# Optimization experiments

Measured on AMD Instinct MI355X. Metric: run time of the kernel, lower is better.

## Reference

```python
import jax, jax.numpy as jnp
import numpy as np

N = 100_000      # nodes
E = 3_200_000    # edges (avg degree 32)
D_IN = 128
D_H = 128
EPS = 1e-12      # F.normalize eps


def setup_inputs() -> dict:
    key = jax.random.key(0)
    k1, k2, k3 = jax.random.split(key, 3)
    X = jax.random.normal(k1, (N, D_IN), dtype=jnp.float32)
    edge_index = jax.random.randint(k2, (2, E), 0, N, dtype=jnp.int32)
    # GCNConv linear weight (stored as [in, out] for X @ W) and bias
    W = jax.random.normal(k3, (D_IN, D_H), dtype=jnp.float32) / np.sqrt(D_IN)
    b = jnp.zeros((D_H,), dtype=jnp.float32)
    # MessageNorm learnable scale, init 1.0
    scale = jnp.ones((1,), dtype=jnp.float32)
    return {"X": X, "edge_index": edge_index, "W": W, "b": b, "scale": scale}


def reference(X, edge_index, W, b, scale):
    n = X.shape[0]
    loop = jnp.arange(n, dtype=edge_index.dtype)
    src = jnp.concatenate([edge_index[0], loop])  # add self loops
    tgt = jnp.concatenate([edge_index[1], loop])
    # symmetric GCN normalization: D^{-1/2} (A+I) D^{-1/2}
    deg = jax.ops.segment_sum(jnp.ones_like(src, X.dtype), tgt, num_segments=n)
    dinv = jnp.where(deg > 0, jax.lax.rsqrt(deg), 0.0)
    norm = dinv[src] * dinv[tgt]  # [E+N]
    XW = X @ W  # [N, D_H]
    msg = jax.ops.segment_sum(norm[:, None] * XW[src], tgt, num_segments=n) + b
    # MessageNorm(learn_scale=True): l2-normalize msg, rescale by ||x||_2 * scale
    msg_n = msg / jnp.maximum(jnp.linalg.norm(msg, axis=-1, keepdims=True), EPS)
    x_norm = jnp.linalg.norm(X, axis=-1, keepdims=True)
    return jax.nn.gelu(msg_n * x_norm * scale, approximate=False)
```

## Files before the change

### kernel.cpp

```cpp
#include <hip/hip_runtime.h>
#include <math.h>

#define D 128
#define NB 391
#define BSH 8
#define BMASK 255
#define CAP 10240
#define EPB 4096
#define LDA 136

typedef unsigned short ushort_t;
typedef unsigned int uint_t;
typedef __attribute__((ext_vector_type(8))) short bfrag;
typedef __attribute__((ext_vector_type(4))) float ffrag;

__device__ inline ushort_t f2bf(float f) {
    uint_t u = __float_as_uint(f);
    uint_t r = (u + 0x7FFFu + ((u >> 16) & 1u)) >> 16;
    return (ushort_t)r;
}

__global__ __launch_bounds__(256) void k_bin(const int* __restrict__ src,
                                             const int* __restrict__ tgt, int e,
                                             int* __restrict__ bucket_cur,
                                             uint_t* __restrict__ binned,
                                             const float* __restrict__ W,
                                             ushort_t* __restrict__ Wt) {
    __shared__ uint_t sval[EPB];
    __shared__ ushort_t sbkt[EPB];
    __shared__ int lcnt[NB];
    __shared__ int lbeg[NB];
    __shared__ int gbase[NB];
    __shared__ int pscan[256];
    int tid = threadIdx.x;

    if (blockIdx.x < 16) {
        int nrow = blockIdx.x * 8 + (tid >> 5);
        int k0 = (tid & 31) * 4;
        ushort4 o;
        o.x = f2bf(W[(size_t)(k0 + 0) * D + nrow]);
        o.y = f2bf(W[(size_t)(k0 + 1) * D + nrow]);
        o.z = f2bf(W[(size_t)(k0 + 2) * D + nrow]);
        o.w = f2bf(W[(size_t)(k0 + 3) * D + nrow]);
        *(ushort4*)&Wt[(size_t)nrow * D + k0] = o;
    }

    int base = blockIdx.x * EPB;
    for (int i = tid; i < NB; i += 256) lcnt[i] = 0;
    __syncthreads();

    int myb[16];
    uint_t myval[16];
#pragma unroll
    for (int k = 0; k < 16; ++k) {
        int i = base + k * 256 + tid;
        if (i < e) {
            int t = tgt[i];
            int s = src[i];
            myb[k] = t >> BSH;
            myval[k] = ((uint_t)s << BSH) | (uint_t)(t & BMASK);
            atomicAdd(&lcnt[myb[k]], 1);
        } else {
            myb[k] = -1;
        }
    }
    __syncthreads();

    int c0 = (2 * tid < NB) ? lcnt[2 * tid] : 0;
    int c1 = (2 * tid + 1 < NB) ? lcnt[2 * tid + 1] : 0;
    int x = c0 + c1;
    pscan[tid] = x;
    __syncthreads();
    for (int off = 1; off < 256; off <<= 1) {
        int y = (tid >= off) ? pscan[tid - off] : 0;
        __syncthreads();
        x += y;
        pscan[tid] = x;
        __syncthreads();
    }
    int pb = x - (c0 + c1);
    if (2 * tid < NB) lbeg[2 * tid] = pb;
    if (2 * tid + 1 < NB) lbeg[2 * tid + 1] = pb + c0;
    __syncthreads();

    for (int i = tid; i < NB; i += 256) {
        int c = lcnt[i];
        gbase[i] = (c > 0) ? atomicAdd(&bucket_cur[i], c) : 0;
        lcnt[i] = lbeg[i];
    }
    __syncthreads();

#pragma unroll
    for (int k = 0; k < 16; ++k) {
        if (myb[k] >= 0) {
            int r = atomicAdd(&lcnt[myb[k]], 1);
            sval[r] = myval[k];
            sbkt[r] = (ushort_t)myb[k];
        }
    }
    __syncthreads();

    int nb = min(e - base, EPB);
    for (int i = tid; i < nb; i += 256) {
        int b = sbkt[i];
        int slot = gbase[b] + (i - lbeg[b]);
        if (slot < CAP) binned[(size_t)b * CAP + slot] = sval[i];
    }
}

__global__ __launch_bounds__(256) void k_sort(const uint_t* __restrict__ binned,
                                              const int* __restrict__ bucket_cur,
                                              int* __restrict__ col,
                                              int* __restrict__ rowptr,
                                              float* __restrict__ dinv, int n) {
    __shared__ uint_t sout[CAP];
    __shared__ int scnt[256];
    __shared__ int sincl[256];
    __shared__ int sofs[256];
    __shared__ int sred[256];
    int b = blockIdx.x;
    int tid = threadIdx.x;

    int v = 0;
    for (int i = tid; i < b; i += 256) v += min(bucket_cur[i], CAP);
    sred[tid] = v;
    __syncthreads();
    for (int off = 128; off >= 1; off >>= 1) {
        if (tid < off) sred[tid] += sred[tid + off];
        __syncthreads();
    }
    int baseg = sred[0];

    int nb = min(bucket_cur[b], CAP);
    const uint_t* bin = binned + (size_t)b * CAP;

    scnt[tid] = 0;
    __syncthreads();
    for (int i = tid; i < nb; i += 256)
        atomicAdd(&scnt[bin[i] & BMASK], 1);
    __syncthreads();
    int x = scnt[tid];
    sincl[tid] = x;
    __syncthreads();
    for (int off = 1; off < 256; off <<= 1) {
        int y = (tid >= off) ? sincl[tid - off] : 0;
        __syncthreads();
        x += y;
        sincl[tid] = x;
        __syncthreads();
    }
    sofs[tid] = x - scnt[tid];
    int t = (b << BSH) + tid;
    if (t < n) {
        rowptr[t + 1] = baseg + x;
        dinv[t] = rsqrtf((float)scnt[tid] + 1.0f);
    }
    if (b == 0 && tid == 0) rowptr[0] = 0;
    __syncthreads();
    for (int i = tid; i < nb; i += 256) {
        uint_t w = bin[i];
        int r = atomicAdd(&sofs[w & BMASK], 1);
        sout[r] = w >> BSH;
    }
    __syncthreads();
    for (int i = tid; i < nb; i += 256)
        col[baseg + i] = (int)sout[i];
}

__global__ __launch_bounds__(256) void k_gemm(const float* __restrict__ X,
                                              const ushort_t* __restrict__ Wt,
                                              const float* __restrict__ dinv,
                                              ushort_t* __restrict__ Y,
                                              float* __restrict__ xnorm, int n) {
    __shared__ ushort_t As[64 * LDA];
    __shared__ ushort_t Bs[128 * LDA];
    int tid = threadIdx.x;
    int row0 = blockIdx.x * 64;

    for (int i = tid; i < 128 * 16; i += 256) {
        int nr = i >> 4, c = (i & 15) << 3;
        *(uint4*)&Bs[nr * LDA + c] = *(const uint4*)&Wt[(size_t)nr * D + c];
    }

    const float4* X4 = (const float4*)X;
#pragma unroll
    for (int i2 = 0; i2 < 8; ++i2) {
        int item = i2 * 256 + tid;
        int r = item >> 5, c4 = item & 31;
        int gr = row0 + r;
        float4 v = (gr < n) ? X4[(size_t)gr * 32 + c4] : make_float4(0.f, 0.f, 0.f, 0.f);
        ushort4 bv;
        bv.x = f2bf(v.x); bv.y = f2bf(v.y); bv.z = f2bf(v.z); bv.w = f2bf(v.w);
        *(ushort4*)&As[r * LDA + c4 * 4] = bv;
        float s = v.x * v.x + v.y * v.y + v.z * v.z + v.w * v.w;
        s += __shfl_xor(s, 1);
        s += __shfl_xor(s, 2);
        s += __shfl_xor(s, 4);
        s += __shfl_xor(s, 8);
        s += __shfl_xor(s, 16);
        if ((tid & 31) == 0 && gr < n) xnorm[gr] = sqrtf(s);
    }
    __syncthreads();

    int w = tid >> 6;
    int lane = tid & 63;
    int q = lane >> 4;
    int mi = lane & 15;

    bfrag xf[4];
#pragma unroll
    for (int kt = 0; kt < 4; ++kt)
        xf[kt] = *(const bfrag*)&As[(w * 16 + mi) * LDA + kt * 32 + q * 8];

    ffrag acc[8];
#pragma unroll
    for (int nt = 0; nt < 8; ++nt) acc[nt] = (ffrag){0.f, 0.f, 0.f, 0.f};

#pragma unroll
    for (int nt = 0; nt < 8; ++nt) {
#pragma unroll
        for (int kt = 0; kt < 4; ++kt) {
            bfrag wf = *(const bfrag*)&Bs[(nt * 16 + mi) * LDA + kt * 32 + q * 8];
            acc[nt] = __builtin_amdgcn_mfma_f32_16x16x32_bf16(wf, xf[kt], acc[nt], 0, 0, 0);
        }
    }

    __syncthreads();
    int gr = row0 + w * 16 + mi;
    float dv = (gr < n) ? dinv[gr] : 0.f;
#pragma unroll
    for (int nt = 0; nt < 8; ++nt) {
        ushort4 o;
        o.x = f2bf(acc[nt][0] * dv);
        o.y = f2bf(acc[nt][1] * dv);
        o.z = f2bf(acc[nt][2] * dv);
        o.w = f2bf(acc[nt][3] * dv);
        *(ushort4*)&As[(w * 16 + mi) * LDA + nt * 16 + q * 4] = o;
    }
    __syncthreads();

    int row = tid >> 2, seg = tid & 3;
    int grow = row0 + row;
    if (grow < n) {
#pragma unroll
        for (int k2 = 0; k2 < 4; ++k2) {
            uint4 vv = *(const uint4*)&As[row * LDA + seg * 32 + k2 * 8];
            *(uint4*)&Y[(size_t)grow * D + seg * 32 + k2 * 8] = vv;
        }
    }
}

__global__ __launch_bounds__(256) void k_agg(const ushort_t* __restrict__ Y,
                                             const float* __restrict__ xnorm,
                                             const float* __restrict__ dinv,
                                             const int* __restrict__ rowptr,
                                             const int* __restrict__ col,
                                             const float* __restrict__ bias,
                                             const float* __restrict__ scale,
                                             float* __restrict__ out, int n) {
    int t = (blockIdx.x * 256 + threadIdx.x) >> 6;
    int lane = threadIdx.x & 63;
    if (t >= n) return;

    const char* Yb = (const char*)Y;
    uint_t lo4 = (uint_t)lane * 4;

    uint_t p = *(const uint_t*)(Yb + (((uint_t)t << 8) + lo4));
    float a0 = __uint_as_float(p << 16);
    float a1 = __uint_as_float(p & 0xFFFF0000u);

    int beg = rowptr[t];
    int end = rowptr[t + 1];
    for (int base = beg; base < end; base += 64) {
        int m = min(end - base, 64);
        uint_t cv = (uint_t)col[base + min(lane, m - 1)];
        int k = 0;
        for (; k + 16 <= m; k += 16) {
            uint_t qv[16];
#pragma unroll
            for (int j = 0; j < 16; ++j) {
                uint_t s = (uint_t)__builtin_amdgcn_readlane((int)cv, k + j);
                qv[j] = *(const uint_t*)(Yb + ((size_t)s << 8) + lo4);
            }
#pragma unroll
            for (int j = 0; j < 16; ++j) {
                a0 += __uint_as_float(qv[j] << 16);
                a1 += __uint_as_float(qv[j] & 0xFFFF0000u);
            }
        }
        for (; k + 4 <= m; k += 4) {
            uint_t qv[4];
#pragma unroll
            for (int j = 0; j < 4; ++j) {
                uint_t s = (uint_t)__builtin_amdgcn_readlane((int)cv, k + j);
                qv[j] = *(const uint_t*)(Yb + ((size_t)s << 8) + lo4);
            }
#pragma unroll
            for (int j = 0; j < 4; ++j) {
                a0 += __uint_as_float(qv[j] << 16);
                a1 += __uint_as_float(qv[j] & 0xFFFF0000u);
            }
        }
        for (; k < m; ++k) {
            uint_t s = (uint_t)__builtin_amdgcn_readlane((int)cv, k);
            uint_t q = *(const uint_t*)(Yb + ((size_t)s << 8) + lo4);
            a0 += __uint_as_float(q << 16);
            a1 += __uint_as_float(q & 0xFFFF0000u);
        }
    }

    float dt = dinv[t];
    float m0 = fmaf(dt, a0, bias[lane * 2]);
    float m1 = fmaf(dt, a1, bias[lane * 2 + 1]);

    float m2 = m0 * m0 + m1 * m1;
#pragma unroll
    for (int m = 32; m >= 1; m >>= 1) m2 += __shfl_xor(m2, m);

    float denom = fmaxf(sqrtf(m2), 1e-12f);
    float fac = xnorm[t] * scale[0] / denom;
    float g0 = m0 * fac;
    float g1 = m1 * fac;
    float2 o;
    o.x = 0.5f * g0 * (1.0f + erff(g0 * 0.70710678118654752440f));
    o.y = 0.5f * g1 * (1.0f + erff(g1 * 0.70710678118654752440f));
    *(float2*)&out[(size_t)t * D + lane * 2] = o;
}


extern "C" void kernel_launch(void* const* d_in, const int* in_sizes, int n_in,
                              void* d_out, int out_size, void* d_ws, size_t ws_size,
                              hipStream_t stream) {
    const float* X     = (const float*)d_in[0];
    const int*   ei    = (const int*)d_in[1];
    const float* W     = (const float*)d_in[2];
    const float* bias  = (const float*)d_in[3];
    const float* scale = (const float*)d_in[4];
    float* out = (float*)d_out;

    int n = in_sizes[0] / D;
    int e = in_sizes[1] / 2;
    const int* src = ei;
    const int* tgt = ei + e;

    char* ws = (char*)d_ws;
    ushort_t* Y = (ushort_t*)ws;   ws += (size_t)n * D * sizeof(ushort_t);
    uint_t* binned = (uint_t*)Y;
    float* dinv = (float*)ws;      ws += (size_t)n * sizeof(float);
    float* xnorm = (float*)ws;     ws += (size_t)n * sizeof(float);
    int* rowptr = (int*)ws;        ws += (size_t)(n + 1) * sizeof(int);
    int* bucket_cur = (int*)ws;    ws += NB * sizeof(int);
    int* col = (int*)ws;           ws += (size_t)e * sizeof(int);
    ushort_t* Wt = (ushort_t*)ws;

    hipMemsetAsync(bucket_cur, 0, NB * sizeof(int), stream);
    k_bin<<<(e + EPB - 1) / EPB, 256, 0, stream>>>(src, tgt, e, bucket_cur, binned, W, Wt);
    k_sort<<<NB, 256, 0, stream>>>(binned, bucket_cur, col, rowptr, dinv, n);
    k_gemm<<<(n + 63) / 64, 256, 0, stream>>>(X, Wt, dinv, Y, xnorm, n);
    k_agg<<<(n + 3) / 4, 256, 0, stream>>>(Y, xnorm, dinv, rowptr, col, bias, scale, out, n);
}
```

Before: 305.9 us.

## Fuse bucket sort and GEMM into one launch, move dinv scaling into aggregation

Merges the per-bucket CSR sort and the X@W GEMM into one kernel, with blocks split by index, so the two independent stages run concurrently and one launch is saved. Because the GEMM no longer waits for dinv, the source-side normalization moves into the aggregation loop as an extra per-edge dinv gather. The global prefix-sum over buckets is dropped: sorted columns are written back in place within each fixed-capacity bucket slice, and each row's begin and end are packed as 16-bit offsets into one int. The cost is an extra random dinv load per edge, a separate binned buffer instead of aliasing Y, and a smaller per-bucket capacity that could overflow on skewed degrees.

```diff
diff --git a/kernel.cpp b/kernel.cpp
--- a/kernel.cpp
+++ b/kernel.cpp
@@ -5,7 +5,7 @@
 #define NB 391
 #define BSH 8
 #define BMASK 255
-#define CAP 10240
+#define CAP 9216
 #define EPB 4096
 #define LDA 136
 
@@ -108,144 +108,130 @@
     }
 }
 
-__global__ __launch_bounds__(256) void k_sort(const uint_t* __restrict__ binned,
-                                              const int* __restrict__ bucket_cur,
-                                              int* __restrict__ col,
-                                              int* __restrict__ rowptr,
-                                              float* __restrict__ dinv, int n) {
-    __shared__ uint_t sout[CAP];
-    __shared__ int scnt[256];
-    __shared__ int sincl[256];
-    __shared__ int sofs[256];
-    __shared__ int sred[256];
-    int b = blockIdx.x;
+__global__ __launch_bounds__(256) void k_mid(uint_t* __restrict__ binned,
+                                             const int* __restrict__ bucket_cur,
+                                             int* __restrict__ rowinfo,
+                                             float* __restrict__ dinv,
+                                             const float* __restrict__ X,
+                                             const ushort_t* __restrict__ Wt,
+                                             ushort_t* __restrict__ Y,
+                                             float* __restrict__ xnorm, int n) {
+    __shared__ __align__(16) char smem[52224];
     int tid = threadIdx.x;
 
-    int v = 0;
-    for (int i = tid; i < b; i += 256) v += min(bucket_cur[i], CAP);
-    sred[tid] = v;
-    __syncthreads();
-    for (int off = 128; off >= 1; off >>= 1) {
-        if (tid < off) sred[tid] += sred[tid + off];
-        __syncthreads();
-    }
-    int baseg = sred[0];
-
-    int nb = min(bucket_cur[b], CAP);
-    const uint_t* bin = binned + (size_t)b * CAP;
-
-    scnt[tid] = 0;
-    __syncthreads();
-    for (int i = tid; i < nb; i += 256)
-        atomicAdd(&scnt[bin[i] & BMASK], 1);
-    __syncthreads();
-    int x = scnt[tid];
-    sincl[tid] = x;
-    __syncthreads();
-    for (int off = 1; off < 256; off <<= 1) {
-        int y = (tid >= off) ? sincl[tid - off] : 0;
-        __syncthreads();
-        x += y;
+    if (blockIdx.x < NB) {
+        uint_t* sout = (uint_t*)smem;
+        int* scnt  = (int*)(smem + CAP * 4);
+        int* sincl = scnt + 256;
+        int* sofs  = sincl + 256;
+        int b = blockIdx.x;
+
+        int nb = min(bucket_cur[b], CAP);
+        uint_t* bin = binned + (size_t)b * CAP;
+
+        scnt[tid] = 0;
+        __syncthreads();
+        for (int i = tid; i < nb; i += 256)
+            atomicAdd(&scnt[bin[i] & BMASK], 1);
+        __syncthreads();
+        int x = scnt[tid];
         sincl[tid] = x;
         __syncthreads();
-    }
-    sofs[tid] = x - scnt[tid];
-    int t = (b << BSH) + tid;
-    if (t < n) {
-        rowptr[t + 1] = baseg + x;
-        dinv[t] = rsqrtf((float)scnt[tid] + 1.0f);
-    }
-    if (b == 0 && tid == 0) rowptr[0] = 0;
-    __syncthreads();
-    for (int i = tid; i < nb; i += 256) {
-        uint_t w = bin[i];
-        int r = atomicAdd(&sofs[w & BMASK], 1);
-        sout[r] = w >> BSH;
-    }
-    __syncthreads();
-    for (int i = tid; i < nb; i += 256)
-        col[baseg + i] = (int)sout[i];
-}
-
-__global__ __launch_bounds__(256) void k_gemm(const float* __restrict__ X,
-                                              const ushort_t* __restrict__ Wt,
-                                              const float* __restrict__ dinv,
-                                              ushort_t* __restrict__ Y,
-                                              float* __restrict__ xnorm, int n) {
-    __shared__ ushort_t As[64 * LDA];
-    __shared__ ushort_t Bs[128 * LDA];
-    int tid = threadIdx.x;
-    int row0 = blockIdx.x * 64;
-
-    for (int i = tid; i < 128 * 16; i += 256) {
-        int nr = i >> 4, c = (i & 15) << 3;
-        *(uint4*)&Bs[nr * LDA + c] = *(const uint4*)&Wt[(size_t)nr * D + c];
-    }
-
-    const float4* X4 = (const float4*)X;
-#pragma unroll
-    for (int i2 = 0; i2 < 8; ++i2) {
-        int item = i2 * 256 + tid;
-        int r = item >> 5, c4 = item & 31;
-        int gr = row0 + r;
-        float4 v = (gr < n) ? X4[(size_t)gr * 32 + c4] : make_float4(0.f, 0.f, 0.f, 0.f);
-        ushort4 bv;
-        bv.x = f2bf(v.x); bv.y = f2bf(v.y); bv.z = f2bf(v.z); bv.w = f2bf(v.w);
-        *(ushort4*)&As[r * LDA + c4 * 4] = bv;
-        float s = v.x * v.x + v.y * v.y + v.z * v.z + v.w * v.w;
-        s += __shfl_xor(s, 1);
-        s += __shfl_xor(s, 2);
-        s += __shfl_xor(s, 4);
-        s += __shfl_xor(s, 8);
-        s += __shfl_xor(s, 16);
-        if ((tid & 31) == 0 && gr < n) xnorm[gr] = sqrtf(s);
-    }
-    __syncthreads();
-
-    int w = tid >> 6;
-    int lane = tid & 63;
-    int q = lane >> 4;
-    int mi = lane & 15;
-
-    bfrag xf[4];
-#pragma unroll
-    for (int kt = 0; kt < 4; ++kt)
-        xf[kt] = *(const bfrag*)&As[(w * 16 + mi) * LDA + kt * 32 + q * 8];
-
-    ffrag acc[8];
-#pragma unroll
-    for (int nt = 0; nt < 8; ++nt) acc[nt] = (ffrag){0.f, 0.f, 0.f, 0.f};
-
-#pragma unroll
-    for (int nt = 0; nt < 8; ++nt) {
-#pragma unroll
-        for (int kt = 0; kt < 4; ++kt) {
-            bfrag wf = *(const bfrag*)&Bs[(nt * 16 + mi) * LDA + kt * 32 + q * 8];
-            acc[nt] = __builtin_amdgcn_mfma_f32_16x16x32_bf16(wf, xf[kt], acc[nt], 0, 0, 0);
-        }
-    }
-
-    __syncthreads();
-    int gr = row0 + w * 16 + mi;
-    float dv = (gr < n) ? dinv[gr] : 0.f;
-#pragma unroll
-    for (int nt = 0; nt < 8; ++nt) {
-        ushort4 o;
-        o.x = f2bf(acc[nt][0] * dv);
-        o.y = f2bf(acc[nt][1] * dv);
-        o.z = f2bf(acc[nt][2] * dv);
-        o.w = f2bf(acc[nt][3] * dv);
-        *(ushort4*)&As[(w * 16 + mi) * LDA + nt * 16 + q * 4] = o;
-    }
-    __syncthreads();
-
-    int row = tid >> 2, seg = tid & 3;
-    int grow = row0 + row;
-    if (grow < n) {
-#pragma unroll
-        for (int k2 = 0; k2 < 4; ++k2) {
-            uint4 vv = *(const uint4*)&As[row * LDA + seg * 32 + k2 * 8];
-            *(uint4*)&Y[(size_t)grow * D + seg * 32 + k2 * 8] = vv;
+        for (int off = 1; off < 256; off <<= 1) {
+            int y = (tid >= off) ? sincl[tid - off] : 0;
+            __syncthreads();
+            x += y;
+            sincl[tid] = x;
+            __syncthreads();
+        }
+        sofs[tid] = x - scnt[tid];
+        int t = (b << BSH) + tid;
+        if (t < n) {
+            rowinfo[t] = ((x - scnt[tid]) << 16) | x;
+            dinv[t] = rsqrtf((float)scnt[tid] + 1.0f);
+        }
+        __syncthreads();
+        for (int i = tid; i < nb; i += 256) {
+            uint_t w = bin[i];
+            int r = atomicAdd(&sofs[w & BMASK], 1);
+            sout[r] = w >> BSH;
+        }
+        __syncthreads();
+        for (int i = tid; i < nb; i += 256)
+            bin[i] = sout[i];
+    } else {
+        ushort_t* As = (ushort_t*)smem;
+        ushort_t* Bs = (ushort_t*)(smem + 17408);
+        int row0 = (blockIdx.x - NB) * 64;
+
+        for (int i = tid; i < 128 * 16; i += 256) {
+            int nr = i >> 4, c = (i & 15) << 3;
+            *(uint4*)&Bs[nr * LDA + c] = *(const uint4*)&Wt[(size_t)nr * D + c];
+        }
+
+        const float4* X4 = (const float4*)X;
+#pragma unroll
+        for (int i2 = 0; i2 < 8; ++i2) {
+            int item = i2 * 256 + tid;
+            int r = item >> 5, c4 = item & 31;
+            int gr = row0 + r;
+            float4 vv = (gr < n) ? X4[(size_t)gr * 32 + c4] : make_float4(0.f, 0.f, 0.f, 0.f);
+            ushort4 bv;
+            bv.x = f2bf(vv.x); bv.y = f2bf(vv.y); bv.z = f2bf(vv.z); bv.w = f2bf(vv.w);
+            *(ushort4*)&As[r * LDA + c4 * 4] = bv;
+            float s = vv.x * vv.x + vv.y * vv.y + vv.z * vv.z + vv.w * vv.w;
+            s += __shfl_xor(s, 1);
+            s += __shfl_xor(s, 2);
+            s += __shfl_xor(s, 4);
+            s += __shfl_xor(s, 8);
+            s += __shfl_xor(s, 16);
+            if ((tid & 31) == 0 && gr < n) xnorm[gr] = sqrtf(s);
+        }
+        __syncthreads();
+
+        int w = tid >> 6;
+        int lane = tid & 63;
+        int q = lane >> 4;
+        int mi = lane & 15;
+
+        bfrag xf[4];
+#pragma unroll
+        for (int kt = 0; kt < 4; ++kt)
+            xf[kt] = *(const bfrag*)&As[(w * 16 + mi) * LDA + kt * 32 + q * 8];
+
+        ffrag acc[8];
+#pragma unroll
+        for (int nt = 0; nt < 8; ++nt) acc[nt] = (ffrag){0.f, 0.f, 0.f, 0.f};
+
+#pragma unroll
+        for (int nt = 0; nt < 8; ++nt) {
+#pragma unroll
+            for (int kt = 0; kt < 4; ++kt) {
+                bfrag wf = *(const bfrag*)&Bs[(nt * 16 + mi) * LDA + kt * 32 + q * 8];
+                acc[nt] = __builtin_amdgcn_mfma_f32_16x16x32_bf16(wf, xf[kt], acc[nt], 0, 0, 0);
+            }
+        }
+
+        __syncthreads();
+#pragma unroll
+        for (int nt = 0; nt < 8; ++nt) {
+            ushort4 o;
+            o.x = f2bf(acc[nt][0]);
+            o.y = f2bf(acc[nt][1]);
+            o.z = f2bf(acc[nt][2]);
+            o.w = f2bf(acc[nt][3]);
+            *(ushort4*)&As[(w * 16 + mi) * LDA + nt * 16 + q * 4] = o;
+        }
+        __syncthreads();
+
+        int row = tid >> 2, seg = tid & 3;
+        int grow = row0 + row;
+        if (grow < n) {
+#pragma unroll
+            for (int k2 = 0; k2 < 4; ++k2) {
+                uint4 vv = *(const uint4*)&As[row * LDA + seg * 32 + k2 * 8];
+                *(uint4*)&Y[(size_t)grow * D + seg * 32 + k2 * 8] = vv;
+            }
         }
     }
 }
@@ -253,8 +239,8 @@
 __global__ __launch_bounds__(256) void k_agg(const ushort_t* __restrict__ Y,
                                              const float* __restrict__ xnorm,
                                              const float* __restrict__ dinv,
-                                             const int* __restrict__ rowptr,
-                                             const int* __restrict__ col,
+                                             const int* __restrict__ rowinfo,
+                                             const uint_t* __restrict__ binned,
                                              const float* __restrict__ bias,
                                              const float* __restrict__ scale,
                                              float* __restrict__ out, int n) {
@@ -264,52 +250,59 @@
 
     const char* Yb = (const char*)Y;
     uint_t lo4 = (uint_t)lane * 4;
+    float dt = dinv[t];
 
     uint_t p = *(const uint_t*)(Yb + (((uint_t)t << 8) + lo4));
-    float a0 = __uint_as_float(p << 16);
-    float a1 = __uint_as_float(p & 0xFFFF0000u);
-
-    int beg = rowptr[t];
-    int end = rowptr[t + 1];
+    float a0 = dt * __uint_as_float(p << 16);
+    float a1 = dt * __uint_as_float(p & 0xFFFF0000u);
+
+    int ri = rowinfo[t];
+    int slice = (t >> BSH) * CAP;
+    int beg = slice + (ri >> 16);
+    int end = slice + (ri & 0xFFFF);
     for (int base = beg; base < end; base += 64) {
         int m = min(end - base, 64);
-        uint_t cv = (uint_t)col[base + min(lane, m - 1)];
+        uint_t cv = binned[base + min(lane, m - 1)];
         int k = 0;
         for (; k + 16 <= m; k += 16) {
             uint_t qv[16];
+            float dv[16];
 #pragma unroll
             for (int j = 0; j < 16; ++j) {
-                uint_t s = (uint_t)__builtin_amdgcn_readlane((int)cv, k + j);
-                qv[j] = *(const uint_t*)(Yb + ((size_t)s << 8) + lo4);
+                int s = __builtin_amdgcn_readlane((int)cv, k + j);
+                dv[j] = dinv[s];
+                qv[j] = *(const uint_t*)(Yb + ((size_t)(uint_t)s << 8) + lo4);
             }
 #pragma unroll
             for (int j = 0; j < 16; ++j) {
-                a0 += __uint_as_float(qv[j] << 16);
-                a1 += __uint_as_float(qv[j] & 0xFFFF0000u);
+                a0 = fmaf(dv[j], __uint_as_float(qv[j] << 16), a0);
+                a1 = fmaf(dv[j], __uint_as_float(qv[j] & 0xFFFF0000u), a1);
             }
         }
         for (; k + 4 <= m; k += 4) {
             uint_t qv[4];
+            float dv[4];
 #pragma unroll
             for (int j = 0; j < 4; ++j) {
-                uint_t s = (uint_t)__builtin_amdgcn_readlane((int)cv, k + j);
-                qv[j] = *(const uint_t*)(Yb + ((size_t)s << 8) + lo4);
+                int s = __builtin_amdgcn_readlane((int)cv, k + j);
+                dv[j] = dinv[s];
+                qv[j] = *(const uint_t*)(Yb + ((size_t)(uint_t)s << 8) + lo4);
             }
 #pragma unroll
             for (int j = 0; j < 4; ++j) {
-                a0 += __uint_as_float(qv[j] << 16);
-                a1 += __uint_as_float(qv[j] & 0xFFFF0000u);
+                a0 = fmaf(dv[j], __uint_as_float(qv[j] << 16), a0);
+                a1 = fmaf(dv[j], __uint_as_float(qv[j] & 0xFFFF0000u), a1);
             }
         }
         for (; k < m; ++k) {
-            uint_t s = (uint_t)__builtin_amdgcn_readlane((int)cv, k);
-            uint_t q = *(const uint_t*)(Yb + ((size_t)s << 8) + lo4);
-            a0 += __uint_as_float(q << 16);
-            a1 += __uint_as_float(q & 0xFFFF0000u);
-        }
-    }
-
-    float dt = dinv[t];
+            int s = __builtin_amdgcn_readlane((int)cv, k);
+            float dvs = dinv[s];
+            uint_t q = *(const uint_t*)(Yb + ((size_t)(uint_t)s << 8) + lo4);
+            a0 = fmaf(dvs, __uint_as_float(q << 16), a0);
+            a1 = fmaf(dvs, __uint_as_float(q & 0xFFFF0000u), a1);
+        }
+    }
+
     float m0 = fmaf(dt, a0, bias[lane * 2]);
     float m1 = fmaf(dt, a1, bias[lane * 2 + 1]);
 
@@ -345,17 +338,17 @@
 
     char* ws = (char*)d_ws;
     ushort_t* Y = (ushort_t*)ws;   ws += (size_t)n * D * sizeof(ushort_t);
-    uint_t* binned = (uint_t*)Y;
+    uint_t* binned = (uint_t*)ws;  ws += (size_t)NB * CAP * sizeof(uint_t);
     float* dinv = (float*)ws;      ws += (size_t)n * sizeof(float);
     float* xnorm = (float*)ws;     ws += (size_t)n * sizeof(float);
-    int* rowptr = (int*)ws;        ws += (size_t)(n + 1) * sizeof(int);
+    int* rowinfo = (int*)ws;       ws += (size_t)n * sizeof(int);
     int* bucket_cur = (int*)ws;    ws += NB * sizeof(int);
-    int* col = (int*)ws;           ws += (size_t)e * sizeof(int);
     ushort_t* Wt = (ushort_t*)ws;
+
+    int ngemm = (n + 63) / 64;
 
     hipMemsetAsync(bucket_cur, 0, NB * sizeof(int), stream);
     k_bin<<<(e + EPB - 1) / EPB, 256, 0, stream>>>(src, tgt, e, bucket_cur, binned, W, Wt);
-    k_sort<<<NB, 256, 0, stream>>>(binned, bucket_cur, col, rowptr, dinv, n);
-    k_gemm<<<(n + 63) / 64, 256, 0, stream>>>(X, Wt, dinv, Y, xnorm, n);
-    k_agg<<<(n + 3) / 4, 256, 0, stream>>>(Y, xnorm, dinv, rowptr, col, bias, scale, out, n);
-}
+    k_mid<<<NB + ngemm, 256, 0, stream>>>(binned, bucket_cur, rowinfo, dinv, X, Wt, Y, xnorm, n);
+    k_agg<<<(n + 3) / 4, 256, 0, stream>>>(Y, xnorm, dinv, rowinfo, binned, bias, scale, out, n);
+}
```

Result: faster. 288.4 us (-5.7%).
